# Performance work log

Measured on AMD Instinct MI355X. Metric: run time of the kernel, lower is better.

The kernel has to match this reference:

```python
import jax, jax.numpy as jnp
import numpy as np

TEMP = 1.0  # softmax temperature from init_kwargs
NEG_BIG = -1e8


def setup_inputs() -> dict:
    key = jax.random.key(0)
    ks = jax.random.split(key, 7)
    T, S, B, H, C, M = 128, 128, 32, 512, 512, 256
    return {
        "hid": jax.random.normal(ks[0], (T, B, H), dtype=jnp.float32),
        "ctx": jax.random.normal(ks[1], (S, B, C), dtype=jnp.float32),
        "ctx_mask": jnp.ones((S, B), dtype=jnp.float32),
        "W_hid2mid": jax.random.normal(ks[2], (M, H), dtype=jnp.float32) * 0.05,
        "W_ctx2mid": jax.random.normal(ks[3], (M, C), dtype=jnp.float32) * 0.05,
        "w_ff": jax.random.normal(ks[4], (M,), dtype=jnp.float32) * 0.05,
        "W_att2hid": jax.random.normal(ks[5], (H, C), dtype=jnp.float32) * 0.05,
    }


def reference(hid, ctx, ctx_mask, W_hid2mid, W_ctx2mid, w_ff, W_att2hid):
    # hid: (T,B,H)  ctx: (S,B,C)  ctx_mask: (S,B)
    hid_m = jnp.einsum('tbh,mh->tbm', hid, W_hid2mid)   # (T,B,M)
    ctx_m = jnp.einsum('sbc,mc->sbm', ctx, W_ctx2mid)   # (S,B,M)
    # broadcast-add -> (S,T,B,M), tanh, project with ff (mid->1), -> scores (S,B,T)
    summed = jnp.tanh(hid_m[None, :, :, :] + ctx_m[:, None, :, :])
    scores = jnp.einsum('stbm,m->sbt', summed, w_ff) / TEMP
    # masked_fill where ctx_mask == 0
    scores = jnp.where(ctx_mask[:, :, None] > 0, scores, NEG_BIG)
    alpha = jax.nn.softmax(scores, axis=0)              # (S,B,T), softmax over S
    attended = jnp.einsum('sbt,sbc->tbc', alpha, ctx)   # (T,B,C)
    z_t = jnp.einsum('tbc,hc->tbh', attended, W_att2hid)  # (T,B,H)
    # torch returns alpha.permute(1,2,0) of (B,T,S) => (T,S,B)
    return (jnp.transpose(alpha, (2, 0, 1)), z_t)
```

## Files before the change

### kernel.cpp

```cpp
#include <hip/hip_runtime.h>
#include <hip/hip_bf16.h>

#define T_DIM 128
#define S_DIM 128
#define B_DIM 32
#define H_DIM 512
#define C_DIM 512
#define M_DIM 256
#define NEG_BIG -1e8f
#define K2LOG2E 2.8853900817779268f

typedef __attribute__((ext_vector_type(8))) short shortx8;
typedef __attribute__((ext_vector_type(4))) float floatx4;

__device__ __forceinline__ unsigned bfpair(float a, float b) {
  unsigned ua = __builtin_bit_cast(unsigned, a); ua += 0x7fffu + ((ua >> 16) & 1u);
  unsigned ub = __builtin_bit_cast(unsigned, b); ub += 0x7fffu + ((ub >> 16) & 1u);
  return (ua >> 16) | (ub & 0xffff0000u);
}
__device__ __forceinline__ uint4 pack2(const float4& a, const float4& b) {
  uint4 o;
  o.x = bfpair(a.x, a.y); o.y = bfpair(a.z, a.w);
  o.z = bfpair(b.x, b.y); o.w = bfpair(b.z, b.w);
  return o;
}
__device__ __forceinline__ ushort bf1(float a) {
  unsigned ua = __builtin_bit_cast(unsigned, a); ua += 0x7fffu + ((ua >> 16) & 1u);
  return (ushort)(ua >> 16);
}

#define GLDS(G, L)                                                        \
  __builtin_amdgcn_global_load_lds(                                       \
      (const __attribute__((address_space(1))) unsigned int*)(G),         \
      (__attribute__((address_space(3))) unsigned int*)(L), 16, 0, 0)

__device__ __forceinline__ void cvt8(const float* __restrict__ s,
                                     ushort* __restrict__ d, int g) {
  const float4 x = *(const float4*)(s + (size_t)g * 8);
  const float4 y = *(const float4*)(s + (size_t)g * 8 + 4);
  uint4 o;
  o.x = bfpair(x.x, x.y); o.y = bfpair(x.z, x.w);
  o.z = bfpair(y.x, y.y); o.w = bfpair(y.z, y.w);
  *(uint4*)(d + (size_t)g * 8) = o;
}

__global__ __launch_bounds__(256) void cvt_kernel(
    const float* a0, ushort* b0, int c0, const float* a1, ushort* b1, int c1,
    const float* a2, ushort* b2, int c2, const float* a3, ushort* b3, int c3,
    const float* a4, ushort* b4, int c4) {
  int g = blockIdx.x * 256 + threadIdx.x;
  if (g < c0) { cvt8(a0, b0, g); return; } g -= c0;
  if (g < c1) { cvt8(a1, b1, g); return; } g -= c1;
  if (g < c2) { cvt8(a2, b2, g); return; } g -= c2;
  if (g < c3) { cvt8(a3, b3, g); return; } g -= c3;
  if (g < c4) { cvt8(a4, b4, g); }
}

__global__ __launch_bounds__(256) void gemm_multi(
    const ushort* __restrict__ HB, const ushort* __restrict__ WhB, float* __restrict__ EH,
    const ushort* __restrict__ CB, const ushort* __restrict__ WcB, float* __restrict__ EC,
    const ushort* __restrict__ WaB, ushort* __restrict__ CWT) {
  __shared__ ushort Xs[2][4096];
  __shared__ ushort Ws[2][4096];
  const int tid = threadIdx.x;
  const int bid = blockIdx.x;

  const ushort *X, *W;
  int n0, m0;
  if (bid < 512) {
    const int lb = bid & 255;
    n0 = (lb >> 2) << 6; m0 = (lb & 3) << 6;
    X = (bid < 256) ? HB : CB;
    W = (bid < 256) ? WhB : WcB;
  } else {
    const int lb = bid - 512;
    n0 = (lb >> 3) << 6;
    m0 = (lb & 7) << 6;
    X = CB;
    W = WaB;
  }

  const int lane = tid & 63, wave = tid >> 6;
  const int wn = wave & 1, wm = wave >> 1;
  const int l15 = lane & 15, lhi = lane >> 4;

  const int row0 = wave * 16 + (lane >> 3);
  const int row1 = row0 + 8;
  const int slot = (lane & 7) ^ (lane >> 3);
  const ushort* xg0 = X + (size_t)(n0 + row0) * 512 + slot * 8;
  const ushort* xg1 = X + (size_t)(n0 + row1) * 512 + slot * 8;
  const ushort* wg0 = W + (size_t)(m0 + row0) * 512 + slot * 8;
  const ushort* wg1 = W + (size_t)(m0 + row1) * 512 + slot * 8;
  const int lb0 = wave * 1024;
  const int lb1 = wave * 1024 + 512;

#define STAGE(NB)                       \
  {                                     \
    GLDS(xg0, &Xs[NB][lb0]);            \
    GLDS(xg1, &Xs[NB][lb1]);            \
    GLDS(wg0, &Ws[NB][lb0]);            \
    GLDS(wg1, &Ws[NB][lb1]);            \
    xg0 += 64; xg1 += 64;               \
    wg0 += 64; wg1 += 64;               \
  }

  floatx4 acc[2][2];
#pragma unroll
  for (int i = 0; i < 2; ++i)
#pragma unroll
    for (int j = 0; j < 2; ++j) acc[i][j] = (floatx4){0.f, 0.f, 0.f, 0.f};

  STAGE(0)
  __syncthreads();
  int cur = 0;

  for (int it = 0; it < 8; ++it) {
    if (it < 7) STAGE(cur ^ 1)
#pragma unroll
    for (int ks = 0; ks < 2; ++ks) {
      const int slotr = lhi + (ks << 2);
      const int sws = ((slotr ^ (l15 & 7)) << 4);
      shortx8 af[2], bfr[2];
#pragma unroll
      for (int fi = 0; fi < 2; ++fi)
        af[fi] = *(const shortx8*)((const char*)&Xs[cur][0] + (wn * 32 + fi * 16 + l15) * 128 + sws);
#pragma unroll
      for (int fj = 0; fj < 2; ++fj)
        bfr[fj] = *(const shortx8*)((const char*)&Ws[cur][0] + (wm * 32 + fj * 16 + l15) * 128 + sws);
#pragma unroll
      for (int fi = 0; fi < 2; ++fi)
#pragma unroll
        for (int fj = 0; fj < 2; ++fj)
          acc[fi][fj] = __builtin_amdgcn_mfma_f32_16x16x32_bf16(af[fi], bfr[fj], acc[fi][fj], 0, 0, 0);
    }
    __syncthreads();
    cur ^= 1;
  }
#undef STAGE

  if (bid < 512) {
    float* Y = (bid < 256) ? EH : EC;
#pragma unroll
    for (int fi = 0; fi < 2; ++fi)
#pragma unroll
      for (int fj = 0; fj < 2; ++fj)
#pragma unroll
        for (int r = 0; r < 4; ++r) {
          const int row = n0 + wn * 32 + fi * 16 + lhi * 4 + r;
          const int col = m0 + wm * 32 + fj * 16 + l15;
          Y[(size_t)row * M_DIM + col] = __builtin_amdgcn_exp2f(K2LOG2E * acc[fi][fj][r]);
        }
  } else {
#pragma unroll
    for (int fi = 0; fi < 2; ++fi)
#pragma unroll
      for (int fj = 0; fj < 2; ++fj)
#pragma unroll
        for (int r = 0; r < 4; ++r) {
          const int row = n0 + wn * 32 + fi * 16 + lhi * 4 + r;
          const int col = m0 + wm * 32 + fj * 16 + l15;
          CWT[(size_t)row * H_DIM + col] = bf1(acc[fi][fj][r]);
        }
  }
}

__global__ __launch_bounds__(256) void zgemm_kernel(
    const float* __restrict__ AWS, const ushort* __restrict__ CWT,
    float* __restrict__ z) {
  __shared__ ushort Xs[4096];
  __shared__ ushort WsT[64 * 72];
  const int tid = threadIdx.x;
  const int m0 = blockIdx.x << 6;
  const int n0 = blockIdx.y << 6;
  const int b = blockIdx.z;
  const int lane = tid & 63, wave = tid >> 6;
  const int wn = wave & 1, wm = wave >> 1;
  const int l15 = lane & 15, lhi = lane >> 4;
  const int r = tid >> 3, c8 = tid & 7;
  const int lr = tid & 63, ls = tid >> 6;
  const int sw0 = (c8 ^ (r & 7)) << 4;
  char* xr0 = (char*)Xs + r * 128 + sw0;
  char* xr1 = (char*)Xs + (r + 32) * 128 + sw0;

  float4 xa[2][2], xb[2][2];
  uint4 wv[2][2];
#pragma unroll
  for (int it = 0; it < 2; ++it) {
    const float* p0 = AWS + ((size_t)(n0 + r) * B_DIM + b) * S_DIM + it * 64 + c8 * 8;
    const float* p1 = AWS + ((size_t)(n0 + r + 32) * B_DIM + b) * S_DIM + it * 64 + c8 * 8;
    xa[it][0] = ((const float4*)p0)[0]; xa[it][1] = ((const float4*)p0)[1];
    xb[it][0] = ((const float4*)p1)[0]; xb[it][1] = ((const float4*)p1)[1];
    const ushort* q = CWT + ((size_t)(it * 64 + lr) * B_DIM + b) * H_DIM + m0 + ls * 8;
    wv[it][0] = *(const uint4*)q;
    wv[it][1] = *(const uint4*)(q + 32);
  }

  floatx4 acc[2][2];
#pragma unroll
  for (int i = 0; i < 2; ++i)
#pragma unroll
    for (int j = 0; j < 2; ++j) acc[i][j] = (floatx4){0.f, 0.f, 0.f, 0.f};

#pragma unroll
  for (int it = 0; it < 2; ++it) {
    __syncthreads();
    *(uint4*)xr0 = pack2(xa[it][0], xa[it][1]);
    *(uint4*)xr1 = pack2(xb[it][0], xb[it][1]);
#pragma unroll
    for (int q = 0; q < 2; ++q) {
      const int hb = ls * 8 + q * 32;
      const ushort* vs = (const ushort*)&wv[it][q];
#pragma unroll
      for (int i = 0; i < 8; ++i) WsT[(hb + i) * 72 + lr] = vs[i];
    }
    __syncthreads();
#pragma unroll
    for (int ks = 0; ks < 2; ++ks) {
      const int slot = lhi + (ks << 2);
      shortx8 af[2], bfr[2];
#pragma unroll
      for (int fi = 0; fi < 2; ++fi) {
        const int row = wn * 32 + fi * 16 + l15;
        af[fi] = *(const shortx8*)((const char*)Xs + row * 128 + ((slot ^ (row & 7)) << 4));
      }
#pragma unroll
      for (int fj = 0; fj < 2; ++fj) {
        const int col = wm * 32 + fj * 16 + l15;
        bfr[fj] = *(const shortx8*)((const char*)WsT + col * 144 + (slot << 4));
      }
#pragma unroll
      for (int fi = 0; fi < 2; ++fi)
#pragma unroll
        for (int fj = 0; fj < 2; ++fj)
          acc[fi][fj] = __builtin_amdgcn_mfma_f32_16x16x32_bf16(af[fi], bfr[fj], acc[fi][fj], 0, 0, 0);
    }
  }

#pragma unroll
  for (int fi = 0; fi < 2; ++fi)
#pragma unroll
    for (int fj = 0; fj < 2; ++fj)
#pragma unroll
      for (int r2 = 0; r2 < 4; ++r2) {
        const int t = n0 + wn * 32 + fi * 16 + lhi * 4 + r2;
        const int h = m0 + wm * 32 + fj * 16 + l15;
        z[((size_t)t * B_DIM + b) * H_DIM + h] = acc[fi][fj][r2];
      }
}

__global__ __launch_bounds__(256) void scores_kernel(
    const float* __restrict__ EH, const float* __restrict__ EC,
    const float* __restrict__ w_ff, const float* __restrict__ ctx_mask,
    float* __restrict__ aws) {
  __shared__ float4 ec[2][8][128];
  __shared__ float4 eh[2][8][8];
  __shared__ float4 wf[2][8];
  __shared__ float msk[S_DIM];
  const int tid = threadIdx.x;
  const int b = blockIdx.y;
  const int t0 = blockIdx.x << 3;
  const int tt = tid >> 6;
  const int st = tid & 63;

  if (tid < S_DIM) msk[tid] = ctx_mask[(size_t)tid * B_DIM + b];

  float4 rec[4], reh, rwf;
#define SLOAD(C)                                                                \
  {                                                                             \
    _Pragma("unroll")                                                           \
    for (int i = 0; i < 4; ++i) {                                               \
      const int idx = tid + (i << 8);                                           \
      const int s_ = idx >> 3, q_ = idx & 7;                                    \
      rec[i] = *(const float4*)(EC + ((size_t)s_ * B_DIM + b) * M_DIM + ((C) << 5) + (q_ << 2)); \
    }                                                                           \
    if (tid < 64)                                                               \
      reh = *(const float4*)(EH + ((size_t)(t0 + (tid >> 3)) * B_DIM + b) * M_DIM + ((C) << 5) + ((tid & 7) << 2)); \
    if (tid < 8) rwf = *(const float4*)(w_ff + ((C) << 5) + (tid << 2));        \
  }
#define SSTORE(BUF)                                                             \
  {                                                                             \
    _Pragma("unroll")                                                           \
    for (int i = 0; i < 4; ++i) {                                               \
      const int idx = tid + (i << 8);                                           \
      ec[BUF][idx & 7][idx >> 3] = rec[i];                                      \
    }                                                                           \
    if (tid < 64) eh[BUF][tid & 7][tid >> 3] = reh;                             \
    if (tid < 8) wf[BUF][tid] = rwf;                                            \
  }

  floatx4 acc[2][2];
#pragma unroll
  for (int i = 0; i < 2; ++i)
#pragma unroll
    for (int j = 0; j < 2; ++j) acc[i][j] = (floatx4){0.f, 0.f, 0.f, 0.f};

  SLOAD(0)
  SSTORE(0)
  __syncthreads();

  for (int c = 0; c < 8; ++c) {
    const int cur = c & 1;
    if (c < 7) SLOAD(c + 1)
#pragma unroll
    for (int q = 0; q < 8; ++q) {
      const float4 w4 = wf[cur][q];
      const float4 e0 = eh[cur][q][2 * tt], e1 = eh[cur][q][2 * tt + 1];
      const float4 c0 = ec[cur][q][st],     c1 = ec[cur][q][st + 64];
#define ACC1(A, E, Cc)                                                 \
  A[0] += w4.x * __builtin_amdgcn_rcpf(E.x * Cc.x + 1.f);              \
  A[1] += w4.y * __builtin_amdgcn_rcpf(E.y * Cc.y + 1.f);              \
  A[2] += w4.z * __builtin_amdgcn_rcpf(E.z * Cc.z + 1.f);              \
  A[3] += w4.w * __builtin_amdgcn_rcpf(E.w * Cc.w + 1.f);
      ACC1(acc[0][0], e0, c0) ACC1(acc[0][1], e0, c1)
      ACC1(acc[1][0], e1, c0) ACC1(acc[1][1], e1, c1)
#undef ACC1
    }
    if (c < 7) {
      SSTORE(cur ^ 1)
      __syncthreads();
    }
  }
#undef SLOAD
#undef SSTORE

  const float mk0 = msk[st], mk1 = msk[st + 64];
  float sc[2][2];
#pragma unroll
  for (int ti = 0; ti < 2; ++ti) {
    const floatx4 a0 = acc[ti][0], a1 = acc[ti][1];
    sc[ti][0] = (mk0 > 0.f) ? -2.f * (a0[0] + a0[1] + a0[2] + a0[3]) : NEG_BIG;
    sc[ti][1] = (mk1 > 0.f) ? -2.f * (a1[0] + a1[1] + a1[2] + a1[3]) : NEG_BIG;
  }
#pragma unroll
  for (int ti = 0; ti < 2; ++ti) {
    float mx = fmaxf(sc[ti][0], sc[ti][1]);
#pragma unroll
    for (int off = 32; off > 0; off >>= 1) mx = fmaxf(mx, __shfl_xor(mx, off));
    const float e0 = __expf(sc[ti][0] - mx), e1 = __expf(sc[ti][1] - mx);
    float sum = e0 + e1;
#pragma unroll
    for (int off = 32; off > 0; off >>= 1) sum += __shfl_xor(sum, off);
    const float rinv = 1.f / sum;
    float* w = aws + ((size_t)(t0 + 2 * tt + ti) * B_DIM + b) * S_DIM;
    w[st] = e0 * rinv;
    w[st + 64] = e1 * rinv;
  }
}

__global__ __launch_bounds__(256) void alpha_tr_kernel(
    const float* __restrict__ aws, float* __restrict__ aout) {
  __shared__ float al[32][129];
  const int t = blockIdx.x;
  const int tid = threadIdx.x;
  {
    const int b_ = tid >> 3, q = tid & 7;
    const float* src = aws + ((size_t)t * B_DIM + b_) * S_DIM + q * 16;
#pragma unroll
    for (int i = 0; i < 4; ++i)
      *(float4*)&al[b_][q * 16 + i * 4] = ((const float4*)src)[i];
  }
  __syncthreads();
  {
    const int s = tid >> 1, half = tid & 1;
    float* dst = aout + ((size_t)t * S_DIM + s) * B_DIM + half * 16;
#pragma unroll
    for (int i = 0; i < 4; ++i) {
      float4 o;
      o.x = al[half * 16 + i * 4 + 0][s];
      o.y = al[half * 16 + i * 4 + 1][s];
      o.z = al[half * 16 + i * 4 + 2][s];
      o.w = al[half * 16 + i * 4 + 3][s];
      ((float4*)dst)[i] = o;
    }
  }
}

extern "C" void kernel_launch(void* const* d_in, const int* in_sizes, int n_in,
                              void* d_out, int out_size, void* d_ws, size_t ws_size,
                              hipStream_t stream) {
  const float* hid       = (const float*)d_in[0];
  const float* ctx       = (const float*)d_in[1];
  const float* ctx_mask  = (const float*)d_in[2];
  const float* W_hid2mid = (const float*)d_in[3];
  const float* W_ctx2mid = (const float*)d_in[4];
  const float* w_ff      = (const float*)d_in[5];
  const float* W_att2hid = (const float*)d_in[6];
  float* out = (float*)d_out;
  float* ws  = (float*)d_ws;

  const size_t MEG = 1 << 20;
  float*  EH  = ws;
  float*  EC  = ws + MEG;
  float*  AWS = ws + 2 * MEG;
  ushort* CWT = (ushort*)(ws + 2 * MEG + MEG / 2);
  ushort* HB  = (ushort*)(ws + 4 * MEG);
  ushort* CB  = (ushort*)(ws + 5 * MEG);
  ushort* WhB = (ushort*)(ws + 6 * MEG);
  ushort* WcB = WhB + 131072;
  ushort* WaB = WcB + 131072;
  float* alpha_out = out;
  float* z_out     = out + T_DIM * S_DIM * B_DIM;

  dim3 blk(256);
  cvt_kernel<<<2304, blk, 0, stream>>>(hid, HB, 262144, ctx, CB, 262144,
                                       W_hid2mid, WhB, 16384, W_ctx2mid, WcB, 16384,
                                       W_att2hid, WaB, 32768);
  gemm_multi<<<1024, blk, 0, stream>>>(HB, WhB, EH, CB, WcB, EC, WaB, CWT);
  scores_kernel<<<dim3(T_DIM / 8, B_DIM), blk, 0, stream>>>(EH, EC, w_ff, ctx_mask, AWS);
  alpha_tr_kernel<<<T_DIM, blk, 0, stream>>>(AWS, alpha_out);
  zgemm_kernel<<<dim3(H_DIM / 64, T_DIM / 64, B_DIM), blk, 0, stream>>>(AWS, CWT, z_out);
}
```

Baseline: 61.15 us.

## Halve scores tile per block and merge alpha transpose with z GEMM launch

```diff
diff --git a/kernel.cpp b/kernel.cpp
--- a/kernel.cpp
+++ b/kernel.cpp
@@ -164,101 +164,17 @@
   }
 }
 
-__global__ __launch_bounds__(256) void zgemm_kernel(
-    const float* __restrict__ AWS, const ushort* __restrict__ CWT,
-    float* __restrict__ z) {
-  __shared__ ushort Xs[4096];
-  __shared__ ushort WsT[64 * 72];
-  const int tid = threadIdx.x;
-  const int m0 = blockIdx.x << 6;
-  const int n0 = blockIdx.y << 6;
-  const int b = blockIdx.z;
-  const int lane = tid & 63, wave = tid >> 6;
-  const int wn = wave & 1, wm = wave >> 1;
-  const int l15 = lane & 15, lhi = lane >> 4;
-  const int r = tid >> 3, c8 = tid & 7;
-  const int lr = tid & 63, ls = tid >> 6;
-  const int sw0 = (c8 ^ (r & 7)) << 4;
-  char* xr0 = (char*)Xs + r * 128 + sw0;
-  char* xr1 = (char*)Xs + (r + 32) * 128 + sw0;
-
-  float4 xa[2][2], xb[2][2];
-  uint4 wv[2][2];
-#pragma unroll
-  for (int it = 0; it < 2; ++it) {
-    const float* p0 = AWS + ((size_t)(n0 + r) * B_DIM + b) * S_DIM + it * 64 + c8 * 8;
-    const float* p1 = AWS + ((size_t)(n0 + r + 32) * B_DIM + b) * S_DIM + it * 64 + c8 * 8;
-    xa[it][0] = ((const float4*)p0)[0]; xa[it][1] = ((const float4*)p0)[1];
-    xb[it][0] = ((const float4*)p1)[0]; xb[it][1] = ((const float4*)p1)[1];
-    const ushort* q = CWT + ((size_t)(it * 64 + lr) * B_DIM + b) * H_DIM + m0 + ls * 8;
-    wv[it][0] = *(const uint4*)q;
-    wv[it][1] = *(const uint4*)(q + 32);
-  }
-
-  floatx4 acc[2][2];
-#pragma unroll
-  for (int i = 0; i < 2; ++i)
-#pragma unroll
-    for (int j = 0; j < 2; ++j) acc[i][j] = (floatx4){0.f, 0.f, 0.f, 0.f};
-
-#pragma unroll
-  for (int it = 0; it < 2; ++it) {
-    __syncthreads();
-    *(uint4*)xr0 = pack2(xa[it][0], xa[it][1]);
-    *(uint4*)xr1 = pack2(xb[it][0], xb[it][1]);
-#pragma unroll
-    for (int q = 0; q < 2; ++q) {
-      const int hb = ls * 8 + q * 32;
-      const ushort* vs = (const ushort*)&wv[it][q];
-#pragma unroll
-      for (int i = 0; i < 8; ++i) WsT[(hb + i) * 72 + lr] = vs[i];
-    }
-    __syncthreads();
-#pragma unroll
-    for (int ks = 0; ks < 2; ++ks) {
-      const int slot = lhi + (ks << 2);
-      shortx8 af[2], bfr[2];
-#pragma unroll
-      for (int fi = 0; fi < 2; ++fi) {
-        const int row = wn * 32 + fi * 16 + l15;
-        af[fi] = *(const shortx8*)((const char*)Xs + row * 128 + ((slot ^ (row & 7)) << 4));
-      }
-#pragma unroll
-      for (int fj = 0; fj < 2; ++fj) {
-        const int col = wm * 32 + fj * 16 + l15;
-        bfr[fj] = *(const shortx8*)((const char*)WsT + col * 144 + (slot << 4));
-      }
-#pragma unroll
-      for (int fi = 0; fi < 2; ++fi)
-#pragma unroll
-        for (int fj = 0; fj < 2; ++fj)
-          acc[fi][fj] = __builtin_amdgcn_mfma_f32_16x16x32_bf16(af[fi], bfr[fj], acc[fi][fj], 0, 0, 0);
-    }
-  }
-
-#pragma unroll
-  for (int fi = 0; fi < 2; ++fi)
-#pragma unroll
-    for (int fj = 0; fj < 2; ++fj)
-#pragma unroll
-      for (int r2 = 0; r2 < 4; ++r2) {
-        const int t = n0 + wn * 32 + fi * 16 + lhi * 4 + r2;
-        const int h = m0 + wm * 32 + fj * 16 + l15;
-        z[((size_t)t * B_DIM + b) * H_DIM + h] = acc[fi][fj][r2];
-      }
-}
-
 __global__ __launch_bounds__(256) void scores_kernel(
     const float* __restrict__ EH, const float* __restrict__ EC,
     const float* __restrict__ w_ff, const float* __restrict__ ctx_mask,
     float* __restrict__ aws) {
   __shared__ float4 ec[2][8][128];
-  __shared__ float4 eh[2][8][8];
+  __shared__ float4 eh[2][8][4];
   __shared__ float4 wf[2][8];
   __shared__ float msk[S_DIM];
   const int tid = threadIdx.x;
   const int b = blockIdx.y;
-  const int t0 = blockIdx.x << 3;
+  const int t0 = blockIdx.x << 2;
   const int tt = tid >> 6;
   const int st = tid & 63;
 
@@ -273,7 +189,7 @@
       const int s_ = idx >> 3, q_ = idx & 7;                                    \
       rec[i] = *(const float4*)(EC + ((size_t)s_ * B_DIM + b) * M_DIM + ((C) << 5) + (q_ << 2)); \
     }                                                                           \
-    if (tid < 64)                                                               \
+    if (tid < 32)                                                               \
       reh = *(const float4*)(EH + ((size_t)(t0 + (tid >> 3)) * B_DIM + b) * M_DIM + ((C) << 5) + ((tid & 7) << 2)); \
     if (tid < 8) rwf = *(const float4*)(w_ff + ((C) << 5) + (tid << 2));        \
   }
@@ -284,15 +200,13 @@
       const int idx = tid + (i << 8);                                           \
       ec[BUF][idx & 7][idx >> 3] = rec[i];                                      \
     }                                                                           \
-    if (tid < 64) eh[BUF][tid & 7][tid >> 3] = reh;                             \
+    if (tid < 32) eh[BUF][tid & 7][tid >> 3] = reh;                             \
     if (tid < 8) wf[BUF][tid] = rwf;                                            \
   }
 
-  floatx4 acc[2][2];
-#pragma unroll
-  for (int i = 0; i < 2; ++i)
-#pragma unroll
-    for (int j = 0; j < 2; ++j) acc[i][j] = (floatx4){0.f, 0.f, 0.f, 0.f};
+  floatx4 acc[2];
+  acc[0] = (floatx4){0.f, 0.f, 0.f, 0.f};
+  acc[1] = (floatx4){0.f, 0.f, 0.f, 0.f};
 
   SLOAD(0)
   SSTORE(0)
@@ -304,15 +218,14 @@
 #pragma unroll
     for (int q = 0; q < 8; ++q) {
       const float4 w4 = wf[cur][q];
-      const float4 e0 = eh[cur][q][2 * tt], e1 = eh[cur][q][2 * tt + 1];
-      const float4 c0 = ec[cur][q][st],     c1 = ec[cur][q][st + 64];
+      const float4 e0 = eh[cur][q][tt];
+      const float4 c0 = ec[cur][q][st], c1 = ec[cur][q][st + 64];
 #define ACC1(A, E, Cc)                                                 \
   A[0] += w4.x * __builtin_amdgcn_rcpf(E.x * Cc.x + 1.f);              \
   A[1] += w4.y * __builtin_amdgcn_rcpf(E.y * Cc.y + 1.f);              \
   A[2] += w4.z * __builtin_amdgcn_rcpf(E.z * Cc.z + 1.f);              \
   A[3] += w4.w * __builtin_amdgcn_rcpf(E.w * Cc.w + 1.f);
-      ACC1(acc[0][0], e0, c0) ACC1(acc[0][1], e0, c1)
-      ACC1(acc[1][0], e1, c0) ACC1(acc[1][1], e1, c1)
+      ACC1(acc[0], e0, c0) ACC1(acc[1], e0, c1)
 #undef ACC1
     }
     if (c < 7) {
@@ -324,55 +237,133 @@
 #undef SSTORE
 
   const float mk0 = msk[st], mk1 = msk[st + 64];
-  float sc[2][2];
-#pragma unroll
-  for (int ti = 0; ti < 2; ++ti) {
-    const floatx4 a0 = acc[ti][0], a1 = acc[ti][1];
-    sc[ti][0] = (mk0 > 0.f) ? -2.f * (a0[0] + a0[1] + a0[2] + a0[3]) : NEG_BIG;
-    sc[ti][1] = (mk1 > 0.f) ? -2.f * (a1[0] + a1[1] + a1[2] + a1[3]) : NEG_BIG;
-  }
-#pragma unroll
-  for (int ti = 0; ti < 2; ++ti) {
-    float mx = fmaxf(sc[ti][0], sc[ti][1]);
-#pragma unroll
-    for (int off = 32; off > 0; off >>= 1) mx = fmaxf(mx, __shfl_xor(mx, off));
-    const float e0 = __expf(sc[ti][0] - mx), e1 = __expf(sc[ti][1] - mx);
-    float sum = e0 + e1;
-#pragma unroll
-    for (int off = 32; off > 0; off >>= 1) sum += __shfl_xor(sum, off);
-    const float rinv = 1.f / sum;
-    float* w = aws + ((size_t)(t0 + 2 * tt + ti) * B_DIM + b) * S_DIM;
-    w[st] = e0 * rinv;
-    w[st + 64] = e1 * rinv;
-  }
-}
-
-__global__ __launch_bounds__(256) void alpha_tr_kernel(
-    const float* __restrict__ aws, float* __restrict__ aout) {
-  __shared__ float al[32][129];
-  const int t = blockIdx.x;
+  const float sc0 = (mk0 > 0.f) ? -2.f * (acc[0][0] + acc[0][1] + acc[0][2] + acc[0][3]) : NEG_BIG;
+  const float sc1 = (mk1 > 0.f) ? -2.f * (acc[1][0] + acc[1][1] + acc[1][2] + acc[1][3]) : NEG_BIG;
+  float mx = fmaxf(sc0, sc1);
+#pragma unroll
+  for (int off = 32; off > 0; off >>= 1) mx = fmaxf(mx, __shfl_xor(mx, off));
+  const float e0 = __expf(sc0 - mx), e1 = __expf(sc1 - mx);
+  float sum = e0 + e1;
+#pragma unroll
+  for (int off = 32; off > 0; off >>= 1) sum += __shfl_xor(sum, off);
+  const float rinv = 1.f / sum;
+  float* w = aws + ((size_t)(t0 + tt) * B_DIM + b) * S_DIM;
+  w[st] = e0 * rinv;
+  w[st + 64] = e1 * rinv;
+}
+
+__global__ __launch_bounds__(256) void epilogue_kernel(
+    const float* __restrict__ AWS, const ushort* __restrict__ CWT,
+    float* __restrict__ z, float* __restrict__ aout) {
+  __shared__ char smem[17408];
   const int tid = threadIdx.x;
-  {
-    const int b_ = tid >> 3, q = tid & 7;
-    const float* src = aws + ((size_t)t * B_DIM + b_) * S_DIM + q * 16;
-#pragma unroll
-    for (int i = 0; i < 4; ++i)
-      *(float4*)&al[b_][q * 16 + i * 4] = ((const float4*)src)[i];
-  }
-  __syncthreads();
-  {
-    const int s = tid >> 1, half = tid & 1;
-    float* dst = aout + ((size_t)t * S_DIM + s) * B_DIM + half * 16;
-#pragma unroll
-    for (int i = 0; i < 4; ++i) {
-      float4 o;
-      o.x = al[half * 16 + i * 4 + 0][s];
-      o.y = al[half * 16 + i * 4 + 1][s];
-      o.z = al[half * 16 + i * 4 + 2][s];
-      o.w = al[half * 16 + i * 4 + 3][s];
-      ((float4*)dst)[i] = o;
-    }
-  }
+
+  if (blockIdx.x >= 512) {
+    float (*al)[129] = (float(*)[129])smem;
+    const int t = blockIdx.x - 512;
+    {
+      const int b_ = tid >> 3, q = tid & 7;
+      const float* src = AWS + ((size_t)t * B_DIM + b_) * S_DIM + q * 16;
+#pragma unroll
+      for (int i = 0; i < 4; ++i)
+        *(float4*)&al[b_][q * 16 + i * 4] = ((const float4*)src)[i];
+    }
+    __syncthreads();
+    {
+      const int s = tid >> 1, half = tid & 1;
+      float* dst = aout + ((size_t)t * S_DIM + s) * B_DIM + half * 16;
+#pragma unroll
+      for (int i = 0; i < 4; ++i) {
+        float4 o;
+        o.x = al[half * 16 + i * 4 + 0][s];
+        o.y = al[half * 16 + i * 4 + 1][s];
+        o.z = al[half * 16 + i * 4 + 2][s];
+        o.w = al[half * 16 + i * 4 + 3][s];
+        ((float4*)dst)[i] = o;
+      }
+    }
+    return;
+  }
+
+  ushort* Xs = (ushort*)smem;
+  ushort* WsT = (ushort*)(smem + 8192);
+  const int bid = blockIdx.x;
+  const int m0 = (bid & 7) << 6;
+  const int n0 = ((bid >> 3) & 1) << 6;
+  const int b = bid >> 4;
+  const int lane = tid & 63, wave = tid >> 6;
+  const int wn = wave & 1, wm = wave >> 1;
+  const int l15 = lane & 15, lhi = lane >> 4;
+  const int r = tid >> 3, c8 = tid & 7;
+  const int lr = tid & 63, ls = tid >> 6;
+  const int sw0 = (c8 ^ (r & 7)) << 4;
+  char* xr0 = (char*)Xs + r * 128 + sw0;
+  char* xr1 = (char*)Xs + (r + 32) * 128 + sw0;
+
+  float4 xa[2][2], xb[2][2];
+  uint4 wv[2][2];
+#pragma unroll
+  for (int it = 0; it < 2; ++it) {
+    const float* p0 = AWS + ((size_t)(n0 + r) * B_DIM + b) * S_DIM + it * 64 + c8 * 8;
+    const float* p1 = AWS + ((size_t)(n0 + r + 32) * B_DIM + b) * S_DIM + it * 64 + c8 * 8;
+    xa[it][0] = ((const float4*)p0)[0]; xa[it][1] = ((const float4*)p0)[1];
+    xb[it][0] = ((const float4*)p1)[0]; xb[it][1] = ((const float4*)p1)[1];
+    const ushort* q = CWT + ((size_t)(it * 64 + lr) * B_DIM + b) * H_DIM + m0 + ls * 8;
+    wv[it][0] = *(const uint4*)q;
+    wv[it][1] = *(const uint4*)(q + 32);
+  }
+
+  floatx4 acc[2][2];
+#pragma unroll
+  for (int i = 0; i < 2; ++i)
+#pragma unroll
+    for (int j = 0; j < 2; ++j) acc[i][j] = (floatx4){0.f, 0.f, 0.f, 0.f};
+
+#pragma unroll
+  for (int it = 0; it < 2; ++it) {
+    __syncthreads();
+    *(uint4*)xr0 = pack2(xa[it][0], xa[it][1]);
+    *(uint4*)xr1 = pack2(xb[it][0], xb[it][1]);
+#pragma unroll
+    for (int q = 0; q < 2; ++q) {
+      const int hb = ls * 8 + q * 32;
+      const ushort* vs = (const ushort*)&wv[it][q];
+#pragma unroll
+      for (int i = 0; i < 8; ++i) WsT[(hb + i) * 72 + lr] = vs[i];
+    }
+    __syncthreads();
+#pragma unroll
+    for (int ks = 0; ks < 2; ++ks) {
+      const int slot = lhi + (ks << 2);
+      shortx8 af[2], bfr[2];
+#pragma unroll
+      for (int fi = 0; fi < 2; ++fi) {
+        const int row = wn * 32 + fi * 16 + l15;
+        af[fi] = *(const shortx8*)((const char*)Xs + row * 128 + ((slot ^ (row & 7)) << 4));
+      }
+#pragma unroll
+      for (int fj = 0; fj < 2; ++fj) {
+        const int col = wm * 32 + fj * 16 + l15;
+        bfr[fj] = *(const shortx8*)((const char*)WsT + col * 144 + (slot << 4));
+      }
+#pragma unroll
+      for (int fi = 0; fi < 2; ++fi)
+#pragma unroll
+        for (int fj = 0; fj < 2; ++fj)
+          acc[fi][fj] = __builtin_amdgcn_mfma_f32_16x16x32_bf16(af[fi], bfr[fj], acc[fi][fj], 0, 0, 0);
+    }
+  }
+
+#pragma unroll
+  for (int fi = 0; fi < 2; ++fi)
+#pragma unroll
+    for (int fj = 0; fj < 2; ++fj)
+#pragma unroll
+      for (int r2 = 0; r2 < 4; ++r2) {
+        const int t = n0 + wn * 32 + fi * 16 + lhi * 4 + r2;
+        const int h = m0 + wm * 32 + fj * 16 + l15;
+        z[((size_t)t * B_DIM + b) * H_DIM + h] = acc[fi][fj][r2];
+      }
 }
 
 extern "C" void kernel_launch(void* const* d_in, const int* in_sizes, int n_in,
@@ -406,7 +397,6 @@
                                        W_hid2mid, WhB, 16384, W_ctx2mid, WcB, 16384,
                                        W_att2hid, WaB, 32768);
   gemm_multi<<<1024, blk, 0, stream>>>(HB, WhB, EH, CB, WcB, EC, WaB, CWT);
-  scores_kernel<<<dim3(T_DIM / 8, B_DIM), blk, 0, stream>>>(EH, EC, w_ff, ctx_mask, AWS);
-  alpha_tr_kernel<<<T_DIM, blk, 0, stream>>>(AWS, alpha_out);
-  zgemm_kernel<<<dim3(H_DIM / 64, T_DIM / 64, B_DIM), blk, 0, stream>>>(AWS, CWT, z_out);
-}
+  scores_kernel<<<dim3(T_DIM / 4, B_DIM), blk, 0, stream>>>(EH, EC, w_ff, ctx_mask, AWS);
+  epilogue_kernel<<<640, blk, 0, stream>>>(AWS, CWT, z_out, alpha_out);
+}
```

New measurement: 64.38 us. +5.3%, slower.

## Fuse activation bf16 conversion into GEMM loads and merge epilogue kernels

Applied to the files above, without the earlier changes.

```diff
diff --git a/kernel.cpp b/kernel.cpp
--- a/kernel.cpp
+++ b/kernel.cpp
@@ -46,37 +46,35 @@
 
 __global__ __launch_bounds__(256) void cvt_kernel(
     const float* a0, ushort* b0, int c0, const float* a1, ushort* b1, int c1,
-    const float* a2, ushort* b2, int c2, const float* a3, ushort* b3, int c3,
-    const float* a4, ushort* b4, int c4) {
+    const float* a2, ushort* b2, int c2) {
   int g = blockIdx.x * 256 + threadIdx.x;
   if (g < c0) { cvt8(a0, b0, g); return; } g -= c0;
   if (g < c1) { cvt8(a1, b1, g); return; } g -= c1;
-  if (g < c2) { cvt8(a2, b2, g); return; } g -= c2;
-  if (g < c3) { cvt8(a3, b3, g); return; } g -= c3;
-  if (g < c4) { cvt8(a4, b4, g); }
+  if (g < c2) { cvt8(a2, b2, g); }
 }
 
 __global__ __launch_bounds__(256) void gemm_multi(
-    const ushort* __restrict__ HB, const ushort* __restrict__ WhB, float* __restrict__ EH,
-    const ushort* __restrict__ CB, const ushort* __restrict__ WcB, float* __restrict__ EC,
+    const float* __restrict__ hid, const ushort* __restrict__ WhB, float* __restrict__ EH,
+    const float* __restrict__ ctx, const ushort* __restrict__ WcB, float* __restrict__ EC,
     const ushort* __restrict__ WaB, ushort* __restrict__ CWT) {
   __shared__ ushort Xs[2][4096];
   __shared__ ushort Ws[2][4096];
   const int tid = threadIdx.x;
   const int bid = blockIdx.x;
 
-  const ushort *X, *W;
+  const float* X;
+  const ushort* W;
   int n0, m0;
   if (bid < 512) {
     const int lb = bid & 255;
     n0 = (lb >> 2) << 6; m0 = (lb & 3) << 6;
-    X = (bid < 256) ? HB : CB;
+    X = (bid < 256) ? hid : ctx;
     W = (bid < 256) ? WhB : WcB;
   } else {
     const int lb = bid - 512;
     n0 = (lb >> 3) << 6;
     m0 = (lb & 7) << 6;
-    X = CB;
+    X = ctx;
     W = WaB;
   }
 
@@ -84,23 +82,32 @@
   const int wn = wave & 1, wm = wave >> 1;
   const int l15 = lane & 15, lhi = lane >> 4;
 
+  const int r = tid >> 3, c8 = tid & 7;
+  const int swx = (c8 ^ (r & 7)) << 4;
+  const float* xp0 = X + (size_t)(n0 + r) * 512 + c8 * 8;
+  const float* xp1 = X + (size_t)(n0 + r + 32) * 512 + c8 * 8;
+
   const int row0 = wave * 16 + (lane >> 3);
   const int row1 = row0 + 8;
   const int slot = (lane & 7) ^ (lane >> 3);
-  const ushort* xg0 = X + (size_t)(n0 + row0) * 512 + slot * 8;
-  const ushort* xg1 = X + (size_t)(n0 + row1) * 512 + slot * 8;
   const ushort* wg0 = W + (size_t)(m0 + row0) * 512 + slot * 8;
   const ushort* wg1 = W + (size_t)(m0 + row1) * 512 + slot * 8;
   const int lb0 = wave * 1024;
   const int lb1 = wave * 1024 + 512;
 
-#define STAGE(NB)                       \
+  float4 xf[4];
+#define LOADX                                        \
+  xf[0] = ((const float4*)xp0)[0];                   \
+  xf[1] = ((const float4*)xp0)[1];                   \
+  xf[2] = ((const float4*)xp1)[0];                   \
+  xf[3] = ((const float4*)xp1)[1];
+#define WRITEX(NB)                                                       \
+  *(uint4*)((char*)&Xs[NB][0] + r * 128 + swx) = pack2(xf[0], xf[1]);    \
+  *(uint4*)((char*)&Xs[NB][0] + (r + 32) * 128 + swx) = pack2(xf[2], xf[3]);
+#define STAGEW(NB)                      \
   {                                     \
-    GLDS(xg0, &Xs[NB][lb0]);            \
-    GLDS(xg1, &Xs[NB][lb1]);            \
     GLDS(wg0, &Ws[NB][lb0]);            \
     GLDS(wg1, &Ws[NB][lb1]);            \
-    xg0 += 64; xg1 += 64;               \
     wg0 += 64; wg1 += 64;               \
   }
 
@@ -110,12 +117,19 @@
 #pragma unroll
     for (int j = 0; j < 2; ++j) acc[i][j] = (floatx4){0.f, 0.f, 0.f, 0.f};
 
-  STAGE(0)
+  LOADX
+  STAGEW(0)
+  WRITEX(0)
   __syncthreads();
   int cur = 0;
 
   for (int it = 0; it < 8; ++it) {
-    if (it < 7) STAGE(cur ^ 1)
+    if (it < 7) {
+      STAGEW(cur ^ 1)
+      xp0 += 64; xp1 += 64;
+      LOADX
+      WRITEX(cur ^ 1)
+    }
 #pragma unroll
     for (int ks = 0; ks < 2; ++ks) {
       const int slotr = lhi + (ks << 2);
@@ -136,7 +150,9 @@
     __syncthreads();
     cur ^= 1;
   }
-#undef STAGE
+#undef LOADX
+#undef WRITEX
+#undef STAGEW
 
   if (bid < 512) {
     float* Y = (bid < 256) ? EH : EC;
@@ -145,10 +161,10 @@
 #pragma unroll
       for (int fj = 0; fj < 2; ++fj)
 #pragma unroll
-        for (int r = 0; r < 4; ++r) {
-          const int row = n0 + wn * 32 + fi * 16 + lhi * 4 + r;
+        for (int rr = 0; rr < 4; ++rr) {
+          const int row = n0 + wn * 32 + fi * 16 + lhi * 4 + rr;
           const int col = m0 + wm * 32 + fj * 16 + l15;
-          Y[(size_t)row * M_DIM + col] = __builtin_amdgcn_exp2f(K2LOG2E * acc[fi][fj][r]);
+          Y[(size_t)row * M_DIM + col] = __builtin_amdgcn_exp2f(K2LOG2E * acc[fi][fj][rr]);
         }
   } else {
 #pragma unroll
@@ -156,96 +172,12 @@
 #pragma unroll
       for (int fj = 0; fj < 2; ++fj)
 #pragma unroll
-        for (int r = 0; r < 4; ++r) {
-          const int row = n0 + wn * 32 + fi * 16 + lhi * 4 + r;
+        for (int rr = 0; rr < 4; ++rr) {
+          const int row = n0 + wn * 32 + fi * 16 + lhi * 4 + rr;
           const int col = m0 + wm * 32 + fj * 16 + l15;
-          CWT[(size_t)row * H_DIM + col] = bf1(acc[fi][fj][r]);
+          CWT[(size_t)row * H_DIM + col] = bf1(acc[fi][fj][rr]);
         }
   }
-}
-
-__global__ __launch_bounds__(256) void zgemm_kernel(
-    const float* __restrict__ AWS, const ushort* __restrict__ CWT,
-    float* __restrict__ z) {
-  __shared__ ushort Xs[4096];
-  __shared__ ushort WsT[64 * 72];
-  const int tid = threadIdx.x;
-  const int m0 = blockIdx.x << 6;
-  const int n0 = blockIdx.y << 6;
-  const int b = blockIdx.z;
-  const int lane = tid & 63, wave = tid >> 6;
-  const int wn = wave & 1, wm = wave >> 1;
-  const int l15 = lane & 15, lhi = lane >> 4;
-  const int r = tid >> 3, c8 = tid & 7;
-  const int lr = tid & 63, ls = tid >> 6;
-  const int sw0 = (c8 ^ (r & 7)) << 4;
-  char* xr0 = (char*)Xs + r * 128 + sw0;
-  char* xr1 = (char*)Xs + (r + 32) * 128 + sw0;
-
-  float4 xa[2][2], xb[2][2];
-  uint4 wv[2][2];
-#pragma unroll
-  for (int it = 0; it < 2; ++it) {
-    const float* p0 = AWS + ((size_t)(n0 + r) * B_DIM + b) * S_DIM + it * 64 + c8 * 8;
-    const float* p1 = AWS + ((size_t)(n0 + r + 32) * B_DIM + b) * S_DIM + it * 64 + c8 * 8;
-    xa[it][0] = ((const float4*)p0)[0]; xa[it][1] = ((const float4*)p0)[1];
-    xb[it][0] = ((const float4*)p1)[0]; xb[it][1] = ((const float4*)p1)[1];
-    const ushort* q = CWT + ((size_t)(it * 64 + lr) * B_DIM + b) * H_DIM + m0 + ls * 8;
-    wv[it][0] = *(const uint4*)q;
-    wv[it][1] = *(const uint4*)(q + 32);
-  }
-
-  floatx4 acc[2][2];
-#pragma unroll
-  for (int i = 0; i < 2; ++i)
-#pragma unroll
-    for (int j = 0; j < 2; ++j) acc[i][j] = (floatx4){0.f, 0.f, 0.f, 0.f};
-
-#pragma unroll
-  for (int it = 0; it < 2; ++it) {
-    __syncthreads();
-    *(uint4*)xr0 = pack2(xa[it][0], xa[it][1]);
-    *(uint4*)xr1 = pack2(xb[it][0], xb[it][1]);
-#pragma unroll
-    for (int q = 0; q < 2; ++q) {
-      const int hb = ls * 8 + q * 32;
-      const ushort* vs = (const ushort*)&wv[it][q];
-#pragma unroll
-      for (int i = 0; i < 8; ++i) WsT[(hb + i) * 72 + lr] = vs[i];
-    }
-    __syncthreads();
-#pragma unroll
-    for (int ks = 0; ks < 2; ++ks) {
-      const int slot = lhi + (ks << 2);
-      shortx8 af[2], bfr[2];
-#pragma unroll
-      for (int fi = 0; fi < 2; ++fi) {
-        const int row = wn * 32 + fi * 16 + l15;
-        af[fi] = *(const shortx8*)((const char*)Xs + row * 128 + ((slot ^ (row & 7)) << 4));
-      }
-#pragma unroll
-      for (int fj = 0; fj < 2; ++fj) {
-        const int col = wm * 32 + fj * 16 + l15;
-        bfr[fj] = *(const shortx8*)((const char*)WsT + col * 144 + (slot << 4));
-      }
-#pragma unroll
-      for (int fi = 0; fi < 2; ++fi)
-#pragma unroll
-        for (int fj = 0; fj < 2; ++fj)
-          acc[fi][fj] = __builtin_amdgcn_mfma_f32_16x16x32_bf16(af[fi], bfr[fj], acc[fi][fj], 0, 0, 0);
-    }
-  }
-
-#pragma unroll
-  for (int fi = 0; fi < 2; ++fi)
-#pragma unroll
-    for (int fj = 0; fj < 2; ++fj)
-#pragma unroll
-      for (int r2 = 0; r2 < 4; ++r2) {
-        const int t = n0 + wn * 32 + fi * 16 + lhi * 4 + r2;
-        const int h = m0 + wm * 32 + fj * 16 + l15;
-        z[((size_t)t * B_DIM + b) * H_DIM + h] = acc[fi][fj][r2];
-      }
 }
 
 __global__ __launch_bounds__(256) void scores_kernel(
@@ -347,32 +279,118 @@
   }
 }
 
-__global__ __launch_bounds__(256) void alpha_tr_kernel(
-    const float* __restrict__ aws, float* __restrict__ aout) {
-  __shared__ float al[32][129];
-  const int t = blockIdx.x;
+__global__ __launch_bounds__(256) void epilogue_kernel(
+    const float* __restrict__ AWS, const ushort* __restrict__ CWT,
+    float* __restrict__ z, float* __restrict__ aout) {
+  __shared__ char smem[17408];
   const int tid = threadIdx.x;
-  {
-    const int b_ = tid >> 3, q = tid & 7;
-    const float* src = aws + ((size_t)t * B_DIM + b_) * S_DIM + q * 16;
-#pragma unroll
-    for (int i = 0; i < 4; ++i)
-      *(float4*)&al[b_][q * 16 + i * 4] = ((const float4*)src)[i];
-  }
-  __syncthreads();
-  {
-    const int s = tid >> 1, half = tid & 1;
-    float* dst = aout + ((size_t)t * S_DIM + s) * B_DIM + half * 16;
-#pragma unroll
-    for (int i = 0; i < 4; ++i) {
-      float4 o;
-      o.x = al[half * 16 + i * 4 + 0][s];
-      o.y = al[half * 16 + i * 4 + 1][s];
-      o.z = al[half * 16 + i * 4 + 2][s];
-      o.w = al[half * 16 + i * 4 + 3][s];
-      ((float4*)dst)[i] = o;
-    }
-  }
+
+  if (blockIdx.x >= 512) {
+    float (*al)[129] = (float(*)[129])smem;
+    const int t = blockIdx.x - 512;
+    {
+      const int b_ = tid >> 3, q = tid & 7;
+      const float* src = AWS + ((size_t)t * B_DIM + b_) * S_DIM + q * 16;
+#pragma unroll
+      for (int i = 0; i < 4; ++i)
+        *(float4*)&al[b_][q * 16 + i * 4] = ((const float4*)src)[i];
+    }
+    __syncthreads();
+    {
+      const int s = tid >> 1, half = tid & 1;
+      float* dst = aout + ((size_t)t * S_DIM + s) * B_DIM + half * 16;
+#pragma unroll
+      for (int i = 0; i < 4; ++i) {
+        float4 o;
+        o.x = al[half * 16 + i * 4 + 0][s];
+        o.y = al[half * 16 + i * 4 + 1][s];
+        o.z = al[half * 16 + i * 4 + 2][s];
+        o.w = al[half * 16 + i * 4 + 3][s];
+        ((float4*)dst)[i] = o;
+      }
+    }
+    return;
+  }
+
+  ushort* Xs = (ushort*)smem;
+  ushort* WsT = (ushort*)(smem + 8192);
+  const int bid = blockIdx.x;
+  const int m0 = (bid & 7) << 6;
+  const int n0 = ((bid >> 3) & 1) << 6;
+  const int b = bid >> 4;
+  const int lane = tid & 63, wave = tid >> 6;
+  const int wn = wave & 1, wm = wave >> 1;
+  const int l15 = lane & 15, lhi = lane >> 4;
+  const int r = tid >> 3, c8 = tid & 7;
+  const int lr = tid & 63, ls = tid >> 6;
+  const int sw0 = (c8 ^ (r & 7)) << 4;
+  char* xr0 = (char*)Xs + r * 128 + sw0;
+  char* xr1 = (char*)Xs + (r + 32) * 128 + sw0;
+
+  float4 xa[2][2], xb[2][2];
+  uint4 wv[2][2];
+#pragma unroll
+  for (int it = 0; it < 2; ++it) {
+    const float* p0 = AWS + ((size_t)(n0 + r) * B_DIM + b) * S_DIM + it * 64 + c8 * 8;
+    const float* p1 = AWS + ((size_t)(n0 + r + 32) * B_DIM + b) * S_DIM + it * 64 + c8 * 8;
+    xa[it][0] = ((const float4*)p0)[0]; xa[it][1] = ((const float4*)p0)[1];
+    xb[it][0] = ((const float4*)p1)[0]; xb[it][1] = ((const float4*)p1)[1];
+    const ushort* q = CWT + ((size_t)(it * 64 + lr) * B_DIM + b) * H_DIM + m0 + ls * 8;
+    wv[it][0] = *(const uint4*)q;
+    wv[it][1] = *(const uint4*)(q + 32);
+  }
+
+  floatx4 acc[2][2];
+#pragma unroll
+  for (int i = 0; i < 2; ++i)
+#pragma unroll
+    for (int j = 0; j < 2; ++j) acc[i][j] = (floatx4){0.f, 0.f, 0.f, 0.f};
+
+#pragma unroll
+  for (int it = 0; it < 2; ++it) {
+    __syncthreads();
+    *(uint4*)xr0 = pack2(xa[it][0], xa[it][1]);
+    *(uint4*)xr1 = pack2(xb[it][0], xb[it][1]);
+#pragma unroll
+    for (int q = 0; q < 2; ++q) {
+      const int hb = ls * 8 + q * 32;
+      const ushort* vs = (const ushort*)&wv[it][q];
+#pragma unroll
+      for (int i = 0; i < 8; ++i) WsT[(hb + i) * 72 + lr] = vs[i];
+    }
+    __syncthreads();
+#pragma unroll
+    for (int ks = 0; ks < 2; ++ks) {
+      const int slot = lhi + (ks << 2);
+      shortx8 af[2], bfr[2];
+#pragma unroll
+      for (int fi = 0; fi < 2; ++fi) {
+        const int row = wn * 32 + fi * 16 + l15;
+        af[fi] = *(const shortx8*)((const char*)Xs + row * 128 + ((slot ^ (row & 7)) << 4));
+      }
+#pragma unroll
+      for (int fj = 0; fj < 2; ++fj) {
+        const int col = wm * 32 + fj * 16 + l15;
+        bfr[fj] = *(const shortx8*)((const char*)WsT + col * 144 + (slot << 4));
+      }
+#pragma unroll
+      for (int fi = 0; fi < 2; ++fi)
+#pragma unroll
+        for (int fj = 0; fj < 2; ++fj)
+          acc[fi][fj] = __builtin_amdgcn_mfma_f32_16x16x32_bf16(af[fi], bfr[fj], acc[fi][fj], 0, 0, 0);
+    }
+  }
+
+#pragma unroll
+  for (int fi = 0; fi < 2; ++fi)
+#pragma unroll
+    for (int fj = 0; fj < 2; ++fj)
+#pragma unroll
+      for (int r2 = 0; r2 < 4; ++r2) {
+        const int t = n0 + wn * 32 + fi * 16 + lhi * 4 + r2;
+        const int h = m0 + wm * 32 + fj * 16 + l15;
+        z[((size_t)t * B_DIM + b) * H_DIM + h] = acc[fi][fj][r2];
+      }
 }
 
 extern "C" void kernel_launch(void* const* d_in, const int* in_sizes, int n_in,
@@ -393,20 +411,17 @@
   float*  EC  = ws + MEG;
   float*  AWS = ws + 2 * MEG;
   ushort* CWT = (ushort*)(ws + 2 * MEG + MEG / 2);
-  ushort* HB  = (ushort*)(ws + 4 * MEG);
-  ushort* CB  = (ushort*)(ws + 5 * MEG);
-  ushort* WhB = (ushort*)(ws + 6 * MEG);
+  ushort* WhB = (ushort*)(ws + 4 * MEG);
   ushort* WcB = WhB + 131072;
   ushort* WaB = WcB + 131072;
   float* alpha_out = out;
   float* z_out     = out + T_DIM * S_DIM * B_DIM;
 
   dim3 blk(256);
-  cvt_kernel<<<2304, blk, 0, stream>>>(hid, HB, 262144, ctx, CB, 262144,
-                                       W_hid2mid, WhB, 16384, W_ctx2mid, WcB, 16384,
-                                       W_att2hid, WaB, 32768);
-  gemm_multi<<<1024, blk, 0, stream>>>(HB, WhB, EH, CB, WcB, EC, WaB, CWT);
+  cvt_kernel<<<256, blk, 0, stream>>>(W_hid2mid, WhB, 16384,
+                                      W_ctx2mid, WcB, 16384,
+                                      W_att2hid, WaB, 32768);
+  gemm_multi<<<1024, blk, 0, stream>>>(hid, WhB, EH, ctx, WcB, EC, WaB, CWT);
   scores_kernel<<<dim3(T_DIM / 8, B_DIM), blk, 0, stream>>>(EH, EC, w_ff, ctx_mask, AWS);
-  alpha_tr_kernel<<<T_DIM, blk, 0, stream>>>(AWS, alpha_out);
-  zgemm_kernel<<<dim3(H_DIM / 64, T_DIM / 64, B_DIM), blk, 0, stream>>>(AWS, CWT, z_out);
-}
+  epilogue_kernel<<<640, blk, 0, stream>>>(AWS, CWT, z_out, alpha_out);
+}
```

Measured after the change: 66.00 us. +7.9%, slower.
